# Kernel optimization log

Measured on AMD Instinct MI355X. Metric: run time of the kernel, lower is better.

Reference implementation:

```python
import jax, jax.numpy as jnp
import numpy as np

N = 100_000      # nodes
E = 1_600_000    # edges (avg degree 16)
F_IN = 128
H = 128
C = 10
G = 2000         # graphs
S = 200          # sets
MAX_SET = G // S # 10; uniform set sizes -> static max_set_size (see notes)


def _linear_init(key, fan_in, fan_out):
    s = 1.0 / np.sqrt(fan_in)
    kw, kb = jax.random.split(key)
    W = jax.random.uniform(kw, (fan_in, fan_out), minval=-s, maxval=s, dtype=jnp.float32)
    b = jax.random.uniform(kb, (fan_out,), minval=-s, maxval=s, dtype=jnp.float32)
    return W, b


def setup_inputs() -> dict:
    key = jax.random.key(0)
    ks = jax.random.split(key, 10)
    x = jax.random.normal(ks[0], (N, F_IN), dtype=jnp.float32)
    edge_index = jax.random.randint(ks[1], (2, E), 0, N, dtype=jnp.int32)
    batch = ((jnp.arange(N) * G) // N).astype(jnp.int32)          # sorted, 50 nodes/graph
    set_batch = (jnp.arange(G) % S).astype(jnp.int32)             # 10 graphs/set
    W1, b1 = _linear_init(ks[2], F_IN, H)
    W2, b2 = _linear_init(ks[3], H, H)
    W3, b3 = _linear_init(ks[4], H, H)
    psiW1, psib1 = _linear_init(ks[5], H, H)
    psiW2, psib2 = _linear_init(ks[6], H, H)
    phiW1, phib1 = _linear_init(ks[7], H, H)
    phiW2, phib2 = _linear_init(ks[8], H, C)
    return dict(x=x, edge_index=edge_index, batch=batch, set_batch=set_batch,
                W1=W1, b1=b1, W2=W2, b2=b2, W3=W3, b3=b3,
                psiW1=psiW1, psib1=psib1, psiW2=psiW2, psib2=psib2,
                phiW1=phiW1, phib1=phib1, phiW2=phiW2, phib2=phib2)


def _gcn_conv(x, src, dst, norm, W, b):
    # GCNConv: out = scatter_add(norm * (xW)[src] -> dst) + b
    h = x @ W
    msg = h[src] * norm[:, None]
    return jax.ops.segment_sum(msg, dst, num_segments=N) + b


def reference(x, edge_index, batch, set_batch,
              W1, b1, W2, b2, W3, b3,
              psiW1, psib1, psiW2, psib2, phiW1, phib1, phiW2, phib2):
    # add self loops, symmetric normalization D^-1/2 (A+I) D^-1/2
    loops = jnp.arange(N, dtype=edge_index.dtype)
    src = jnp.concatenate([edge_index[0], loops])
    dst = jnp.concatenate([edge_index[1], loops])
    deg = jax.ops.segment_sum(jnp.ones(src.shape, x.dtype), dst, num_segments=N)
    dinv = jnp.where(deg > 0, jax.lax.rsqrt(deg), 0.0)
    norm = dinv[src] * dinv[dst]

    h = jax.nn.relu(_gcn_conv(x, src, dst, norm, W1, b1))   # dropout is eval-mode identity
    h = jax.nn.relu(_gcn_conv(h, src, dst, norm, W2, b2))
    h = jax.nn.relu(_gcn_conv(h, src, dst, norm, W3, b3))

    # global mean pool over nodes -> [G, H]
    sums = jax.ops.segment_sum(h, batch, num_segments=G)
    cnts = jax.ops.segment_sum(jnp.ones((N,), h.dtype), batch, num_segments=G)
    graph_emb = sums / jnp.maximum(cnts, 1.0)[:, None]

    # ragged-to-padded pack: [S, MAX_SET, H]
    set_sizes = jax.ops.segment_sum(jnp.ones((G,), jnp.int32), set_batch, num_segments=S)
    offsets = jnp.concatenate([jnp.zeros((1,), jnp.int32), jnp.cumsum(set_sizes)])
    sorted_idx = jnp.argsort(set_batch)                      # stable by default
    positions_sorted = jnp.arange(G, dtype=jnp.int32) - offsets[set_batch[sorted_idx]]
    positions = jnp.zeros((G,), jnp.int32).at[sorted_idx].set(positions_sorted)
    x_pad = jnp.zeros((S, MAX_SET, H), x.dtype).at[set_batch, positions].set(graph_emb)

    # DeepSets: phi(sum_i psi(x_i))
    p = jnp.tanh(jax.nn.relu(x_pad @ psiW1 + psib1) @ psiW2 + psib2)
    agg = p.sum(axis=1)                                      # [S, H]
    return jax.nn.relu(agg @ phiW1 + phib1) @ phiW2 + phib2  # [S, C]
```

## Files before the change

### kernel.cpp

```cpp
#include <hip/hip_runtime.h>
#include <hip/hip_bf16.h>
#include <hip/hip_fp16.h>
#include <math.h>

#define NN 100000
#define EE 1600000
#define HH 128
#define GG 2000
#define SS 200
#define CC 10
#define NPG 50
#define PGS 10
#define NCLS 128
#define CLSW 782
#define EPB 4096
#define NBLKH 391
#define SCAN_N (NCLS * NBLKH)

typedef _Float16 f16x8 __attribute__((ext_vector_type(8)));
typedef float    f32x4 __attribute__((ext_vector_type(4)));



__global__ __launch_bounds__(256) void histo_kernel(const int* __restrict__ ei_dst,
                                                    int* __restrict__ blkcnt) {
    __shared__ int h[4][NCLS];
    for (int i = threadIdx.x; i < 4 * NCLS; i += 256) ((int*)h)[i] = 0;
    __syncthreads();
    int w = threadIdx.x >> 6;
    int base = blockIdx.x * EPB;
#pragma unroll
    for (int i = 0; i < 16; ++i) {
        int idx = base + i * 256 + threadIdx.x;
        if (idx < EE) {
            int d = __builtin_nontemporal_load(ei_dst + idx);
            atomicAdd(&h[w][(unsigned)d / CLSW], 1);
        }
    }
    __syncthreads();
    for (int c = threadIdx.x; c < NCLS; c += 256)
        blkcnt[c * NBLKH + blockIdx.x] = h[0][c] + h[1][c] + h[2][c] + h[3][c];
}

__global__ void scan_chunk_kernel(const int* __restrict__ v, int* __restrict__ outp,
                                  int* __restrict__ bsum, int n) {
    __shared__ int s[256];
    int tid = threadIdx.x;
    int i = blockIdx.x * 256 + tid;
    int x = (i < n) ? v[i] : 0;
    s[tid] = x;
    __syncthreads();
    for (int off = 1; off < 256; off <<= 1) {
        int y = (tid >= off) ? s[tid - off] : 0;
        __syncthreads();
        s[tid] += y;
        __syncthreads();
    }
    if (i < n) outp[i + 1] = s[tid];
    if (tid == 255) bsum[blockIdx.x] = s[255];
}

__global__ void scan_bsums_kernel(int* bsum, int nb) {
    __shared__ int s[512];
    int tid = threadIdx.x;
    int x = (tid < nb) ? bsum[tid] : 0;
    s[tid] = x;
    __syncthreads();
    for (int off = 1; off < 512; off <<= 1) {
        int y = (tid >= off) ? s[tid - off] : 0;
        __syncthreads();
        s[tid] += y;
        __syncthreads();
    }
    if (tid < nb) bsum[tid] = s[tid];
}

__global__ void scan_finish_kernel(int* __restrict__ outp, const int* __restrict__ bsum, int n) {
    int i = blockIdx.x * 256 + threadIdx.x;
    if (i < n) {
        if (blockIdx.x > 0) outp[i + 1] += bsum[blockIdx.x - 1];
    }
    if (i == 0) outp[0] = 0;
}

__global__ __launch_bounds__(256) void scatter_bin_kernel(const int* __restrict__ ei,
                                                          const int* __restrict__ blkoff,
                                                          unsigned int* __restrict__ ebin) {
    __shared__ int cur[NCLS];
    for (int c = threadIdx.x; c < NCLS; c += 256) cur[c] = blkoff[c * NBLKH + blockIdx.x];
    __syncthreads();
    int base = blockIdx.x * EPB;
#pragma unroll
    for (int i = 0; i < 16; ++i) {
        int idx = base + i * 256 + threadIdx.x;
        if (idx < EE) {
            int s = __builtin_nontemporal_load(ei + idx);
            int d = __builtin_nontemporal_load(ei + EE + idx);
            int c = (unsigned)d / CLSW;
            int pos = atomicAdd(&cur[c], 1);
            ebin[pos] = ((unsigned)(d - c * CLSW) << 17) | (unsigned)s;
        }
    }
}

__global__ __launch_bounds__(256) void count_dinv_kernel(const unsigned int* __restrict__ ebin,
                                                         const int* __restrict__ blkoff,
                                                         int* __restrict__ row_ptr,
                                                         float* __restrict__ dinv) {
    __shared__ int cnt[CLSW];
    __shared__ int part[256];
    int c = blockIdx.x;
    for (int i = threadIdx.x; i < CLSW; i += 256) cnt[i] = 0;
    __syncthreads();
    int beg = blkoff[c * NBLKH];
    int end = blkoff[(c + 1) * NBLKH];
    int n0 = c * CLSW;
    for (int k = beg + threadIdx.x; k < end; k += 256) {
        unsigned int e = __builtin_nontemporal_load(ebin + k);
        atomicAdd(&cnt[e >> 17], 1);
    }
    __syncthreads();
    int nn = min(n0 + CLSW, NN) - n0;
    int t = threadIdx.x;
    int base = t * 4;
    int lpre[4];
    int lsum = 0;
#pragma unroll
    for (int i = 0; i < 4; ++i) {
        int idx = base + i;
        int v = (idx < nn) ? cnt[idx] : 0;
        lpre[i] = lsum;
        lsum += v;
    }
    part[t] = lsum;
    __syncthreads();
    for (int off = 1; off < 256; off <<= 1) {
        int y = (t >= off) ? part[t - off] : 0;
        __syncthreads();
        part[t] += y;
        __syncthreads();
    }
    int add = beg + ((t > 0) ? part[t - 1] : 0);
#pragma unroll
    for (int i = 0; i < 4; ++i) {
        int idx = base + i;
        if (idx < nn) {
            row_ptr[n0 + idx] = add + lpre[i];
            dinv[n0 + idx] = 1.0f / sqrtf((float)(cnt[idx] + 1));
        }
    }
    if (t == 0) row_ptr[n0 + nn] = end;
}

__global__ __launch_bounds__(256) void fill_class_kernel(const unsigned int* __restrict__ ebin,
                                                         const int* __restrict__ blkoff,
                                                         const int* __restrict__ row_ptr,
                                                         int* __restrict__ col) {
    __shared__ int cur[CLSW];
    int c = blockIdx.x;
    int n0 = c * CLSW;
    int nn = min(n0 + CLSW, NN) - n0;
    for (int i = threadIdx.x; i < nn; i += 256) cur[i] = row_ptr[n0 + i];
    __syncthreads();
    int beg = blkoff[c * NBLKH];
    int end = blkoff[(c + 1) * NBLKH];
    for (int k = beg + threadIdx.x; k < end; k += 256) {
        unsigned int e = __builtin_nontemporal_load(ebin + k);
        int o = atomicAdd(&cur[e >> 17], 1);
        col[o] = (int)(e & 0x1FFFFu);
    }
}


#define WTP 136

template <bool IN32>
__global__ __launch_bounds__(256) void gemm_mfma_kernel(const void* __restrict__ Xv,
                                                        const float* __restrict__ W,
                                                        const float* __restrict__ dinv,
                                                        _Float16* __restrict__ Y, int nrows) {
    __shared__ _Float16 Wt[128][WTP];
    __shared__ _Float16 Ob[128][WTP];
    int tid = threadIdx.x;
    int row0 = blockIdx.x * 128;

    const float4* W4 = (const float4*)W;
#pragma unroll
    for (int it = 0; it < 16; ++it) {
        int f = it * 256 + tid;
        int k = f >> 5;
        int c = (f & 31) << 2;
        float4 v = W4[f];
        Wt[c + 0][k] = (_Float16)v.x;
        Wt[c + 1][k] = (_Float16)v.y;
        Wt[c + 2][k] = (_Float16)v.z;
        Wt[c + 3][k] = (_Float16)v.w;
    }
    __syncthreads();

    int wave = tid >> 6;
    int l = tid & 63;
    int arow = l & 15;
    int kg = l >> 4;
    int baseRow = row0 + wave * 32;

    f16x8 afrag[2][4];
#pragma unroll
    for (int rt = 0; rt < 2; ++rt) {
        int r = baseRow + rt * 16 + arow;
        r = min(r, nrows - 1);
        if (IN32) {
            const float* xr = ((const float*)Xv) + (size_t)r * 128;
#pragma unroll
            for (int ks = 0; ks < 4; ++ks) {
                int k0 = ks * 32 + kg * 8;
                float4 a = ((const float4*)xr)[k0 >> 2];
                float4 b = ((const float4*)xr)[(k0 >> 2) + 1];
                f16x8 v;
                v[0] = (_Float16)a.x; v[1] = (_Float16)a.y;
                v[2] = (_Float16)a.z; v[3] = (_Float16)a.w;
                v[4] = (_Float16)b.x; v[5] = (_Float16)b.y;
                v[6] = (_Float16)b.z; v[7] = (_Float16)b.w;
                afrag[rt][ks] = v;
            }
        } else {
            const f16x8* xr = (const f16x8*)(((const _Float16*)Xv) + (size_t)r * 128);
#pragma unroll
            for (int ks = 0; ks < 4; ++ks) afrag[rt][ks] = xr[ks * 4 + kg];
        }
    }

    f32x4 acc[2][8];
#pragma unroll
    for (int rt = 0; rt < 2; ++rt)
#pragma unroll
        for (int ct = 0; ct < 8; ++ct) acc[rt][ct] = (f32x4){0.f, 0.f, 0.f, 0.f};

#pragma unroll
    for (int ct = 0; ct < 8; ++ct) {
#pragma unroll
        for (int ks = 0; ks < 4; ++ks) {
            f16x8 b = *(const f16x8*)&Wt[ct * 16 + arow][ks * 32 + kg * 8];
            acc[0][ct] = __builtin_amdgcn_mfma_f32_16x16x32_f16(afrag[0][ks], b, acc[0][ct], 0, 0, 0);
            acc[1][ct] = __builtin_amdgcn_mfma_f32_16x16x32_f16(afrag[1][ks], b, acc[1][ct], 0, 0, 0);
        }
    }

    float dv[2][4];
#pragma unroll
    for (int rt = 0; rt < 2; ++rt)
#pragma unroll
        for (int j = 0; j < 4; ++j) {
            int r = baseRow + rt * 16 + 4 * kg + j;
            dv[rt][j] = dinv[min(r, nrows - 1)];
        }

#pragma unroll
    for (int rt = 0; rt < 2; ++rt)
#pragma unroll
        for (int ct = 0; ct < 8; ++ct)
#pragma unroll
            for (int j = 0; j < 4; ++j)
                Ob[wave * 32 + rt * 16 + 4 * kg + j][ct * 16 + arow] =
                    (_Float16)(acc[rt][ct][j] * dv[rt][j]);

#pragma unroll
    for (int i = 0; i < 8; ++i) {
        int q = i * 64 + l;
        int lrow = q >> 4;
        int c = q & 15;
        int r = baseRow + lrow;
        if (r < nrows) {
            f16x8 v = *(const f16x8*)&Ob[wave * 32 + lrow][c * 8];
            *(f16x8*)(Y + (size_t)r * 128 + c * 8) = v;
        }
    }
}


__global__ __launch_bounds__(256) void aggregate_kernel(const __half* __restrict__ hw,
                                                        const int* __restrict__ rp,
                                                        const int* __restrict__ col,
                                                        const float* __restrict__ dinv,
                                                        const float* __restrict__ bias,
                                                        __half* __restrict__ outp, int n) {
    int wid = threadIdx.x >> 6;
    int lane = threadIdx.x & 63;
    int i = blockIdx.x * 4 + wid;
    if (i >= n) return;
    const __half2* hw2 = (const __half2*)hw;
    float2 a0, a1, a2, a3;
    {
        float2 self = __half22float2(hw2[(size_t)i * 64 + lane]);
        a0.x = self.x; a0.y = self.y;
    }
    a1 = make_float2(0.f, 0.f);
    a2 = make_float2(0.f, 0.f);
    a3 = make_float2(0.f, 0.f);
    int j0 = rp[i], j1 = rp[i + 1];
    int j = j0;
    for (; j + 8 <= j1; j += 8) {
        int s0 = col[j + 0];
        int s1 = col[j + 1];
        int s2 = col[j + 2];
        int s3 = col[j + 3];
        int s4 = col[j + 4];
        int s5 = col[j + 5];
        int s6 = col[j + 6];
        int s7 = col[j + 7];
        __half2 v0 = hw2[(size_t)s0 * 64 + lane];
        __half2 v1 = hw2[(size_t)s1 * 64 + lane];
        __half2 v2 = hw2[(size_t)s2 * 64 + lane];
        __half2 v3 = hw2[(size_t)s3 * 64 + lane];
        __half2 v4 = hw2[(size_t)s4 * 64 + lane];
        __half2 v5 = hw2[(size_t)s5 * 64 + lane];
        __half2 v6 = hw2[(size_t)s6 * 64 + lane];
        __half2 v7 = hw2[(size_t)s7 * 64 + lane];
        float2 f;
        f = __half22float2(v0); a0.x += f.x; a0.y += f.y;
        f = __half22float2(v1); a1.x += f.x; a1.y += f.y;
        f = __half22float2(v2); a2.x += f.x; a2.y += f.y;
        f = __half22float2(v3); a3.x += f.x; a3.y += f.y;
        f = __half22float2(v4); a0.x += f.x; a0.y += f.y;
        f = __half22float2(v5); a1.x += f.x; a1.y += f.y;
        f = __half22float2(v6); a2.x += f.x; a2.y += f.y;
        f = __half22float2(v7); a3.x += f.x; a3.y += f.y;
    }
    for (; j + 4 <= j1; j += 4) {
        int s0 = col[j + 0];
        int s1 = col[j + 1];
        int s2 = col[j + 2];
        int s3 = col[j + 3];
        __half2 v0 = hw2[(size_t)s0 * 64 + lane];
        __half2 v1 = hw2[(size_t)s1 * 64 + lane];
        __half2 v2 = hw2[(size_t)s2 * 64 + lane];
        __half2 v3 = hw2[(size_t)s3 * 64 + lane];
        float2 f;
        f = __half22float2(v0); a0.x += f.x; a0.y += f.y;
        f = __half22float2(v1); a1.x += f.x; a1.y += f.y;
        f = __half22float2(v2); a2.x += f.x; a2.y += f.y;
        f = __half22float2(v3); a3.x += f.x; a3.y += f.y;
    }
    for (; j < j1; ++j) {
        int s = col[j];
        float2 f = __half22float2(hw2[(size_t)s * 64 + lane]);
        a0.x += f.x; a0.y += f.y;
    }
    float di = dinv[i];
    float2 acc;
    acc.x = ((a0.x + a1.x) + (a2.x + a3.x)) * di;
    acc.y = ((a0.y + a1.y) + (a2.y + a3.y)) * di;
    float2 bv = ((const float2*)bias)[lane];
    float rx = fmaxf(acc.x + bv.x, 0.f);
    float ry = fmaxf(acc.y + bv.y, 0.f);
    ((__half2*)outp)[(size_t)i * 64 + lane] = __floats2half2_rn(rx, ry);
}


__global__ __launch_bounds__(256) void pool_kernel(const __half* __restrict__ h,
                                                   float* __restrict__ gemb) {
    int wid = threadIdx.x >> 6;
    int lane = threadIdx.x & 63;
    int g = blockIdx.x * 4 + wid;
    if (g >= GG) return;
    const __half2* h2 = (const __half2*)h;
    float2 acc = {0.f, 0.f};
    size_t base = (size_t)g * NPG * 64;
    for (int r = 0; r < NPG; ++r) {
        float2 v = __half22float2(h2[base + (size_t)r * 64 + lane]);
        acc.x += v.x;
        acc.y += v.y;
    }
    float2 o;
    o.x = acc.x / (float)NPG;
    o.y = acc.y / (float)NPG;
    ((float2*)gemb)[(size_t)g * 64 + lane] = o;
}


__global__ __launch_bounds__(128) void psi_kernel(const float* __restrict__ gemb,
                                                  const float* __restrict__ W1,
                                                  const float* __restrict__ b1,
                                                  const float* __restrict__ W2,
                                                  const float* __restrict__ b2,
                                                  float* __restrict__ pbuf) {
    __shared__ float e[128];
    __shared__ float t[128];
    int g = blockIdx.x;
    int c = threadIdx.x;
    e[c] = gemb[(size_t)g * 128 + c];
    __syncthreads();
    float acc = b1[c];
#pragma unroll 8
    for (int k = 0; k < 128; ++k) acc += e[k] * W1[k * 128 + c];
    t[c] = fmaxf(acc, 0.f);
    __syncthreads();
    float acc2 = b2[c];
#pragma unroll 8
    for (int k = 0; k < 128; ++k) acc2 += t[k] * W2[k * 128 + c];
    pbuf[(size_t)g * 128 + c] = tanhf(acc2);
}


__global__ __launch_bounds__(128) void phi_kernel(const float* __restrict__ pbuf,
                                                  const float* __restrict__ W1,
                                                  const float* __restrict__ b1,
                                                  const float* __restrict__ W2,
                                                  const float* __restrict__ b2,
                                                  float* __restrict__ out) {
    __shared__ float a[128];
    __shared__ float u[128];
    int s = blockIdx.x;
    int c = threadIdx.x;
    float acc = 0.f;
#pragma unroll
    for (int p = 0; p < PGS; ++p) acc += pbuf[(size_t)(s + p * SS) * 128 + c];
    a[c] = acc;
    __syncthreads();
    float acc1 = b1[c];
#pragma unroll 8
    for (int k = 0; k < 128; ++k) acc1 += a[k] * W1[k * 128 + c];
    u[c] = fmaxf(acc1, 0.f);
    __syncthreads();
    if (c < CC) {
        float acc2 = b2[c];
#pragma unroll 8
        for (int k = 0; k < 128; ++k) acc2 += u[k] * W2[k * CC + c];
        out[(size_t)s * CC + c] = acc2;
    }
}


extern "C" void kernel_launch(void* const* d_in, const int* in_sizes, int n_in,
                              void* d_out, int out_size, void* d_ws, size_t ws_size,
                              hipStream_t stream) {
    const float* x   = (const float*)d_in[0];
    const int* ei    = (const int*)d_in[1];
    const float* W1  = (const float*)d_in[4];
    const float* b1  = (const float*)d_in[5];
    const float* W2  = (const float*)d_in[6];
    const float* b2  = (const float*)d_in[7];
    const float* W3  = (const float*)d_in[8];
    const float* b3  = (const float*)d_in[9];
    const float* pW1 = (const float*)d_in[10];
    const float* pb1 = (const float*)d_in[11];
    const float* pW2 = (const float*)d_in[12];
    const float* pb2 = (const float*)d_in[13];
    const float* fW1 = (const float*)d_in[14];
    const float* fb1 = (const float*)d_in[15];
    const float* fW2 = (const float*)d_in[16];
    const float* fb2 = (const float*)d_in[17];
    float* out = (float*)d_out;

    char* p = (char*)d_ws;
    auto alloc = [&](size_t bytes) {
        char* r = p;
        p += (bytes + 255) & ~(size_t)255;
        return r;
    };
    float*        dinv    = (float*)alloc((size_t)NN * 4);
    int*          row_ptr = (int*)alloc((size_t)(NN + 1) * 4);
    int*          bsum2   = (int*)alloc(512 * 4);
    int*          blkcnt  = (int*)alloc((size_t)SCAN_N * 4);
    int*          blkoff  = (int*)alloc((size_t)(SCAN_N + 1) * 4);
    int*          col     = (int*)alloc((size_t)EE * 4);
    unsigned int* ebin    = (unsigned int*)alloc((size_t)EE * 4);
    _Float16*     bufA    = (_Float16*)alloc((size_t)NN * HH * 2);
    __half*       bufB    = (__half*)alloc((size_t)NN * HH * 2);
    float*        gemb    = (float*)alloc((size_t)GG * HH * 4);
    float*        pbuf    = (float*)alloc((size_t)GG * HH * 4);

    const int nblkS = (SCAN_N + 255) / 256;

    histo_kernel<<<NBLKH, 256, 0, stream>>>(ei + EE, blkcnt);
    scan_chunk_kernel<<<nblkS, 256, 0, stream>>>(blkcnt, blkoff, bsum2, SCAN_N);
    scan_bsums_kernel<<<1, 512, 0, stream>>>(bsum2, nblkS);
    scan_finish_kernel<<<nblkS, 256, 0, stream>>>(blkoff, bsum2, SCAN_N);
    scatter_bin_kernel<<<NBLKH, 256, 0, stream>>>(ei, blkoff, ebin);
    count_dinv_kernel<<<NCLS, 256, 0, stream>>>(ebin, blkoff, row_ptr, dinv);
    fill_class_kernel<<<NCLS, 256, 0, stream>>>(ebin, blkoff, row_ptr, col);

    const int gemmBlocks = (NN + 127) / 128;
    const int aggBlocks  = (NN + 3) / 4;

    gemm_mfma_kernel<true><<<gemmBlocks, 256, 0, stream>>>(x, W1, dinv, bufA, NN);
    aggregate_kernel<<<aggBlocks, 256, 0, stream>>>((const __half*)bufA, row_ptr, col, dinv, b1, bufB, NN);
    gemm_mfma_kernel<false><<<gemmBlocks, 256, 0, stream>>>(bufB, W2, dinv, bufA, NN);
    aggregate_kernel<<<aggBlocks, 256, 0, stream>>>((const __half*)bufA, row_ptr, col, dinv, b2, bufB, NN);
    gemm_mfma_kernel<false><<<gemmBlocks, 256, 0, stream>>>(bufB, W3, dinv, bufA, NN);
    aggregate_kernel<<<aggBlocks, 256, 0, stream>>>((const __half*)bufA, row_ptr, col, dinv, b3, bufB, NN);

    pool_kernel<<<(GG + 3) / 4, 256, 0, stream>>>(bufB, gemb);
    psi_kernel<<<GG, 128, 0, stream>>>(gemb, pW1, pb1, pW2, pb2, pbuf);
    phi_kernel<<<SS, 128, 0, stream>>>(pbuf, fW1, fb1, fW2, fb2, out);
}
```

Measured before the change: 374.9 us.

## Pre-transpose GEMM weights, widen aggregate unroll, fuse pool with psi

Adds a small kernel that converts and transposes W1..W3 to fp16 once, so each GEMM block reads B fragments straight from global memory instead of rebuilding a shared-memory copy per block. The aggregate kernel's main loop is unrolled to 16 neighbours to keep more gathers in flight. Pooling and the psi MLP are merged into one kernel, which drops the gemb round trip and one launch. In exchange, B fragments now come from global/L2 rather than LDS, and the 16-wide loop raises register use and sends degree-16 nodes with fewer than 16 neighbours to the 4-wide and scalar tails.

```diff
diff --git a/kernel.cpp b/kernel.cpp
--- a/kernel.cpp
+++ b/kernel.cpp
@@ -172,31 +172,34 @@
 }
 
 
+__global__ __launch_bounds__(256) void wt_kernel(const float* __restrict__ W1,
+                                                 const float* __restrict__ W2,
+                                                 const float* __restrict__ W3,
+                                                 _Float16* __restrict__ wt) {
+    int m = blockIdx.y;
+    const float* W = (m == 0) ? W1 : ((m == 1) ? W2 : W3);
+    _Float16* o = wt + (size_t)m * 16384;
+    int f = blockIdx.x * 256 + threadIdx.x;
+    float4 v = ((const float4*)W)[f];
+    int k = f >> 5;
+    int c = (f & 31) << 2;
+    o[(c + 0) * 128 + k] = (_Float16)v.x;
+    o[(c + 1) * 128 + k] = (_Float16)v.y;
+    o[(c + 2) * 128 + k] = (_Float16)v.z;
+    o[(c + 3) * 128 + k] = (_Float16)v.w;
+}
+
+
 #define WTP 136
 
 template <bool IN32>
 __global__ __launch_bounds__(256) void gemm_mfma_kernel(const void* __restrict__ Xv,
-                                                        const float* __restrict__ W,
+                                                        const _Float16* __restrict__ Wt,
                                                         const float* __restrict__ dinv,
                                                         _Float16* __restrict__ Y, int nrows) {
-    __shared__ _Float16 Wt[128][WTP];
     __shared__ _Float16 Ob[128][WTP];
     int tid = threadIdx.x;
     int row0 = blockIdx.x * 128;
-
-    const float4* W4 = (const float4*)W;
-#pragma unroll
-    for (int it = 0; it < 16; ++it) {
-        int f = it * 256 + tid;
-        int k = f >> 5;
-        int c = (f & 31) << 2;
-        float4 v = W4[f];
-        Wt[c + 0][k] = (_Float16)v.x;
-        Wt[c + 1][k] = (_Float16)v.y;
-        Wt[c + 2][k] = (_Float16)v.z;
-        Wt[c + 3][k] = (_Float16)v.w;
-    }
-    __syncthreads();
 
     int wave = tid >> 6;
     int l = tid & 63;
@@ -240,7 +243,7 @@
     for (int ct = 0; ct < 8; ++ct) {
 #pragma unroll
         for (int ks = 0; ks < 4; ++ks) {
-            f16x8 b = *(const f16x8*)&Wt[ct * 16 + arow][ks * 32 + kg * 8];
+            f16x8 b = *(const f16x8*)(Wt + (size_t)(ct * 16 + arow) * 128 + ks * 32 + kg * 8);
             acc[0][ct] = __builtin_amdgcn_mfma_f32_16x16x32_f16(afrag[0][ks], b, acc[0][ct], 0, 0, 0);
             acc[1][ct] = __builtin_amdgcn_mfma_f32_16x16x32_f16(afrag[1][ks], b, acc[1][ct], 0, 0, 0);
         }
@@ -299,7 +302,7 @@
     a3 = make_float2(0.f, 0.f);
     int j0 = rp[i], j1 = rp[i + 1];
     int j = j0;
-    for (; j + 8 <= j1; j += 8) {
+    for (; j + 16 <= j1; j += 16) {
         int s0 = col[j + 0];
         int s1 = col[j + 1];
         int s2 = col[j + 2];
@@ -308,6 +311,14 @@
         int s5 = col[j + 5];
         int s6 = col[j + 6];
         int s7 = col[j + 7];
+        int s8 = col[j + 8];
+        int s9 = col[j + 9];
+        int s10 = col[j + 10];
+        int s11 = col[j + 11];
+        int s12 = col[j + 12];
+        int s13 = col[j + 13];
+        int s14 = col[j + 14];
+        int s15 = col[j + 15];
         __half2 v0 = hw2[(size_t)s0 * 64 + lane];
         __half2 v1 = hw2[(size_t)s1 * 64 + lane];
         __half2 v2 = hw2[(size_t)s2 * 64 + lane];
@@ -316,15 +327,31 @@
         __half2 v5 = hw2[(size_t)s5 * 64 + lane];
         __half2 v6 = hw2[(size_t)s6 * 64 + lane];
         __half2 v7 = hw2[(size_t)s7 * 64 + lane];
+        __half2 v8 = hw2[(size_t)s8 * 64 + lane];
+        __half2 v9 = hw2[(size_t)s9 * 64 + lane];
+        __half2 v10 = hw2[(size_t)s10 * 64 + lane];
+        __half2 v11 = hw2[(size_t)s11 * 64 + lane];
+        __half2 v12 = hw2[(size_t)s12 * 64 + lane];
+        __half2 v13 = hw2[(size_t)s13 * 64 + lane];
+        __half2 v14 = hw2[(size_t)s14 * 64 + lane];
+        __half2 v15 = hw2[(size_t)s15 * 64 + lane];
         float2 f;
-        f = __half22float2(v0); a0.x += f.x; a0.y += f.y;
-        f = __half22float2(v1); a1.x += f.x; a1.y += f.y;
-        f = __half22float2(v2); a2.x += f.x; a2.y += f.y;
-        f = __half22float2(v3); a3.x += f.x; a3.y += f.y;
-        f = __half22float2(v4); a0.x += f.x; a0.y += f.y;
-        f = __half22float2(v5); a1.x += f.x; a1.y += f.y;
-        f = __half22float2(v6); a2.x += f.x; a2.y += f.y;
-        f = __half22float2(v7); a3.x += f.x; a3.y += f.y;
+        f = __half22float2(v0);  a0.x += f.x; a0.y += f.y;
+        f = __half22float2(v1);  a1.x += f.x; a1.y += f.y;
+        f = __half22float2(v2);  a2.x += f.x; a2.y += f.y;
+        f = __half22float2(v3);  a3.x += f.x; a3.y += f.y;
+        f = __half22float2(v4);  a0.x += f.x; a0.y += f.y;
+        f = __half22float2(v5);  a1.x += f.x; a1.y += f.y;
+        f = __half22float2(v6);  a2.x += f.x; a2.y += f.y;
+        f = __half22float2(v7);  a3.x += f.x; a3.y += f.y;
+        f = __half22float2(v8);  a0.x += f.x; a0.y += f.y;
+        f = __half22float2(v9);  a1.x += f.x; a1.y += f.y;
+        f = __half22float2(v10); a2.x += f.x; a2.y += f.y;
+        f = __half22float2(v11); a3.x += f.x; a3.y += f.y;
+        f = __half22float2(v12); a0.x += f.x; a0.y += f.y;
+        f = __half22float2(v13); a1.x += f.x; a1.y += f.y;
+        f = __half22float2(v14); a2.x += f.x; a2.y += f.y;
+        f = __half22float2(v15); a3.x += f.x; a3.y += f.y;
     }
     for (; j + 4 <= j1; j += 4) {
         int s0 = col[j + 0];
@@ -357,48 +384,52 @@
 }
 
 
-__global__ __launch_bounds__(256) void pool_kernel(const __half* __restrict__ h,
-                                                   float* __restrict__ gemb) {
-    int wid = threadIdx.x >> 6;
-    int lane = threadIdx.x & 63;
-    int g = blockIdx.x * 4 + wid;
-    if (g >= GG) return;
-    const __half2* h2 = (const __half2*)h;
-    float2 acc = {0.f, 0.f};
-    size_t base = (size_t)g * NPG * 64;
-    for (int r = 0; r < NPG; ++r) {
-        float2 v = __half22float2(h2[base + (size_t)r * 64 + lane]);
-        acc.x += v.x;
-        acc.y += v.y;
-    }
-    float2 o;
-    o.x = acc.x / (float)NPG;
-    o.y = acc.y / (float)NPG;
-    ((float2*)gemb)[(size_t)g * 64 + lane] = o;
-}
-
-
-__global__ __launch_bounds__(128) void psi_kernel(const float* __restrict__ gemb,
-                                                  const float* __restrict__ W1,
-                                                  const float* __restrict__ b1,
-                                                  const float* __restrict__ W2,
-                                                  const float* __restrict__ b2,
-                                                  float* __restrict__ pbuf) {
+__global__ __launch_bounds__(256) void poolpsi_kernel(const __half* __restrict__ h,
+                                                      const float* __restrict__ W1,
+                                                      const float* __restrict__ b1,
+                                                      const float* __restrict__ W2,
+                                                      const float* __restrict__ b2,
+                                                      float* __restrict__ pbuf) {
+    __shared__ float2 part[4][64];
     __shared__ float e[128];
     __shared__ float t[128];
     int g = blockIdx.x;
+    int q = threadIdx.x & 63;
+    int rg = threadIdx.x >> 6;
+    const __half2* h2 = (const __half2*)h;
+    size_t base = (size_t)g * NPG * 64;
+    float2 acc = {0.f, 0.f};
+    for (int r = rg; r < NPG; r += 4) {
+        float2 v = __half22float2(h2[base + (size_t)r * 64 + q]);
+        acc.x += v.x;
+        acc.y += v.y;
+    }
+    part[rg][q] = acc;
+    __syncthreads();
+    if (threadIdx.x < 64) {
+        float2 s0 = part[0][threadIdx.x];
+        float2 s1 = part[1][threadIdx.x];
+        float2 s2 = part[2][threadIdx.x];
+        float2 s3 = part[3][threadIdx.x];
+        e[2 * threadIdx.x]     = ((s0.x + s1.x) + (s2.x + s3.x)) * (1.0f / NPG);
+        e[2 * threadIdx.x + 1] = ((s0.y + s1.y) + (s2.y + s3.y)) * (1.0f / NPG);
+    }
+    __syncthreads();
     int c = threadIdx.x;
-    e[c] = gemb[(size_t)g * 128 + c];
-    __syncthreads();
-    float acc = b1[c];
+    float acc1 = 0.f, acc2 = 0.f;
+    if (c < 128) {
+        acc1 = b1[c];
 #pragma unroll 8
-    for (int k = 0; k < 128; ++k) acc += e[k] * W1[k * 128 + c];
-    t[c] = fmaxf(acc, 0.f);
-    __syncthreads();
-    float acc2 = b2[c];
+        for (int k = 0; k < 128; ++k) acc1 += e[k] * W1[k * 128 + c];
+        t[c] = fmaxf(acc1, 0.f);
+    }
+    __syncthreads();
+    if (c < 128) {
+        acc2 = b2[c];
 #pragma unroll 8
-    for (int k = 0; k < 128; ++k) acc2 += t[k] * W2[k * 128 + c];
-    pbuf[(size_t)g * 128 + c] = tanhf(acc2);
+        for (int k = 0; k < 128; ++k) acc2 += t[k] * W2[k * 128 + c];
+        pbuf[(size_t)g * 128 + c] = tanhf(acc2);
+    }
 }
 
 
@@ -465,12 +496,14 @@
     int*          blkoff  = (int*)alloc((size_t)(SCAN_N + 1) * 4);
     int*          col     = (int*)alloc((size_t)EE * 4);
     unsigned int* ebin    = (unsigned int*)alloc((size_t)EE * 4);
+    _Float16*     wtbuf   = (_Float16*)alloc((size_t)3 * 16384 * 2);
     _Float16*     bufA    = (_Float16*)alloc((size_t)NN * HH * 2);
     __half*       bufB    = (__half*)alloc((size_t)NN * HH * 2);
-    float*        gemb    = (float*)alloc((size_t)GG * HH * 4);
     float*        pbuf    = (float*)alloc((size_t)GG * HH * 4);
 
     const int nblkS = (SCAN_N + 255) / 256;
+
+    wt_kernel<<<dim3(16, 3), 256, 0, stream>>>(W1, W2, W3, wtbuf);
 
     histo_kernel<<<NBLKH, 256, 0, stream>>>(ei + EE, blkcnt);
     scan_chunk_kernel<<<nblkS, 256, 0, stream>>>(blkcnt, blkoff, bsum2, SCAN_N);
@@ -483,14 +516,13 @@
     const int gemmBlocks = (NN + 127) / 128;
     const int aggBlocks  = (NN + 3) / 4;
 
-    gemm_mfma_kernel<true><<<gemmBlocks, 256, 0, stream>>>(x, W1, dinv, bufA, NN);
+    gemm_mfma_kernel<true><<<gemmBlocks, 256, 0, stream>>>(x, wtbuf, dinv, bufA, NN);
     aggregate_kernel<<<aggBlocks, 256, 0, stream>>>((const __half*)bufA, row_ptr, col, dinv, b1, bufB, NN);
-    gemm_mfma_kernel<false><<<gemmBlocks, 256, 0, stream>>>(bufB, W2, dinv, bufA, NN);
+    gemm_mfma_kernel<false><<<gemmBlocks, 256, 0, stream>>>(bufB, wtbuf + 16384, dinv, bufA, NN);
     aggregate_kernel<<<aggBlocks, 256, 0, stream>>>((const __half*)bufA, row_ptr, col, dinv, b2, bufB, NN);
-    gemm_mfma_kernel<false><<<gemmBlocks, 256, 0, stream>>>(bufB, W3, dinv, bufA, NN);
+    gemm_mfma_kernel<false><<<gemmBlocks, 256, 0, stream>>>(bufB, wtbuf + 32768, dinv, bufA, NN);
     aggregate_kernel<<<aggBlocks, 256, 0, stream>>>((const __half*)bufA, row_ptr, col, dinv, b3, bufB, NN);
 
-    pool_kernel<<<(GG + 3) / 4, 256, 0, stream>>>(bufB, gemb);
-    psi_kernel<<<GG, 128, 0, stream>>>(gemb, pW1, pb1, pW2, pb2, pbuf);
+    poolpsi_kernel<<<GG, 256, 0, stream>>>(bufB, pW1, pb1, pW2, pb2, pbuf);
     phi_kernel<<<SS, 128, 0, stream>>>(pbuf, fW1, fb1, fW2, fb2, out);
 }
```

Result: slower. 389.6 us (+3.9%).
